# Kernel tuning notes

Measured on AMD Instinct MI355X. Metric: run time of the kernel, lower is better.

The kernel has to match this reference:

```python
import jax, jax.numpy as jnp
import numpy as np

N_NODES = 120000
EM = 128
N_EDGES = 1920000
BS = 1024
L = 10

def setup_inputs() -> dict:
    key = jax.random.key(0)
    ks = jax.random.split(key, 24)
    stdv = 1.0 / np.sqrt(EM)
    u = lambda k, shape: jax.random.uniform(k, shape, jnp.float32, -stdv, stdv)
    return {
        'src': jax.random.randint(ks[0], (N_EDGES,), 0, N_NODES, jnp.int32),
        'dst': jax.random.randint(ks[1], (N_EDGES,), 0, N_NODES, jnp.int32),
        'user': jax.random.randint(ks[2], (BS, 1), 0, 20000, jnp.int32),
        'seq': jax.random.randint(ks[3], (BS, L), 0, 100000, jnp.int32),
        'mask': jnp.ones((BS, L), jnp.float32),
        'seq_len': jax.random.randint(ks[4], (BS,), 1, L, jnp.int32),
        'pos_idx': jax.random.randint(ks[5], (BS, L), 0, 200, jnp.int32),
        'item_num': 100000,
        'v2e': u(ks[6], (N_NODES, EM)),
        'W_self': u(ks[7], (EM, EM)),
        'W_neigh': u(ks[8], (EM, EM)),
        'sage_b': u(ks[9], (EM,)),
        'pos_emb': u(ks[10], (200, EM)),
        'w1': u(ks[11], (2 * EM, EM)),
        'w2': u(ks[12], (EM, 1)),
        'glu1_w': u(ks[13], (EM, EM)),
        'glu1_b': u(ks[14], (EM,)),
        'glu2_w': u(ks[15], (EM, EM)),
        'w3': u(ks[16], (EM, EM)),
        'w4': u(ks[17], (EM, 1)),
        'glu3_w': u(ks[18], (EM, EM)),
        'glu3_b': u(ks[19], (EM,)),
        'glu4_w': u(ks[20], (EM, EM)),
        'sc_w': u(ks[21], (2 * EM, 1)),
        'sc_b': u(ks[22], (1,)),
    }


def reference(src, dst, user, seq, mask, seq_len, pos_idx, item_num,
              v2e, W_self, W_neigh, sage_b, pos_emb,
              w1, w2, glu1_w, glu1_b, glu2_w,
              w3, w4, glu3_w, glu3_b, glu4_w, sc_w, sc_b):
    N = v2e.shape[0]
    # SAGEConv 'mean': fc_self(x) + fc_neigh(mean over in-neighbors) + bias, then ReLU
    deg = jax.ops.segment_sum(jnp.ones_like(dst, jnp.float32), dst, num_segments=N)
    agg = jax.ops.segment_sum(v2e[src], dst, num_segments=N)
    agg = agg / jnp.clip(deg, 1.0)[:, None]
    h1 = jax.nn.relu(v2e @ W_self + agg @ W_neigh + sage_b)

    u_idx = user + item_num                      # [bs,1]
    node_embeds = (h1[seq] + v2e[seq]) * 0.5     # [bs,L,em]
    user_embeds = (h1[u_idx] + v2e[u_idx]) * 0.5 # [bs,1,em]
    seq_embeds = user_embeds[:, 0]               # [bs,em]

    m = mask[..., None]                          # [bs,L,1]
    # compute_hidden_vector (GLU-gated attention with positional embedding)
    pe = pos_emb[pos_idx]                        # [bs,L,em]
    tmp = jnp.sum(node_embeds * m, axis=1) / jnp.sum(m, axis=1)  # masked mean [bs,em]
    hs = tmp[:, None, :]
    nh = jnp.tanh(jnp.concatenate([pe, node_embeds], -1) @ w1)
    nh = jax.nn.sigmoid(nh @ glu1_w + glu1_b + hs @ glu2_w)
    beta = (nh @ w2) * m
    sess_vec = jnp.sum(beta * node_embeds, axis=1)  # [bs,em]

    # sess_user_vector
    nh2 = jnp.tanh(node_embeds @ w3)
    nh2 = jax.nn.sigmoid(nh2 @ glu3_w + glu3_b + user_embeds @ glu4_w)
    beta2 = (nh2 @ w4) * m
    sess_user = jnp.sum(beta2 * node_embeds, axis=1)  # [bs,em]

    alpha = jax.nn.sigmoid(jnp.concatenate([sess_vec, sess_user], 1) @ sc_w + sc_b)  # [bs,1]
    seq_embeds = seq_embeds + alpha * sess_vec + (1.0 - alpha) * sess_user

    scores = seq_embeds @ v2e[1:].T              # [bs, N-1]
    return scores
```

## Files before the change

### kernel.cpp

```cpp
#include <hip/hip_runtime.h>
#include <stdint.h>

#define N_NODES   120000
#define EM        128
#define N_EDGES_C 1920000
#define BSZ       1024
#define SL        10
#define N_GATHER  (BSZ*SL + BSZ)
#define N_OUTCOL  (N_NODES - 1)
#define NBLK_E    1875
#define CHUNK_E   1024
#define NPANEL    938
#define NBLK_S    (NPANEL*8)

typedef __attribute__((ext_vector_type(8))) short bf16x8;
typedef __attribute__((ext_vector_type(4))) float f32x4;

#define GLOBAL_AS __attribute__((address_space(1)))
#define LDS_AS    __attribute__((address_space(3)))

__device__ inline void gload_lds16(const void* g, void* l) {
  __builtin_amdgcn_global_load_lds((const GLOBAL_AS unsigned int*)g,
                                   (LDS_AS unsigned int*)l, 16, 0, 0);
}

__device__ inline unsigned pk_bf16(float a, float b) {
  unsigned ua = __builtin_bit_cast(unsigned, a);
  ua += 0x7fffu + ((ua >> 16) & 1u);
  unsigned ub = __builtin_bit_cast(unsigned, b);
  ub += 0x7fffu + ((ub >> 16) & 1u);
  return (ua >> 16) | (ub & 0xffff0000u);
}

__device__ inline float bf2f(unsigned short u) {
  return __builtin_bit_cast(float, ((unsigned)u) << 16);
}

#define MAP_OFF   0u
#define CNT_OFF   480000u
#define DEG_OFF   480256u
#define OFFS_OFF  525312u
#define CUR_OFF   570368u
#define AGG_OFF   615424u
#define SORT_OFF  21742592u
#define NE_OFF    29422592u
#define UE_OFF    34665472u
#define SB_OFF    35189760u
#define V2EB_OFF  37748736u

__global__ __launch_bounds__(256) void k_init(int* __restrict__ ws_ints) {
  int t = blockIdx.x*256 + threadIdx.x;
  ws_ints[t] = (t < N_NODES) ? -1 : 0;
}

__global__ __launch_bounds__(256) void k_tobf16(const float* __restrict__ v2e,
    unsigned short* __restrict__ v2eb) {
  size_t base = ((size_t)blockIdx.x*256 + threadIdx.x) * 8;
  float4 v0 = *(const float4*)(v2e + base);
  float4 v1 = *(const float4*)(v2e + base + 4);
  uint4 o;
  o.x = pk_bf16(v0.x, v0.y); o.y = pk_bf16(v0.z, v0.w);
  o.z = pk_bf16(v1.x, v1.y); o.w = pk_bf16(v1.z, v1.w);
  *(uint4*)(v2eb + base) = o;
}

__global__ __launch_bounds__(256) void k_assign(const int* __restrict__ seq,
    const int* __restrict__ user, const int* __restrict__ item_num,
    int* __restrict__ map, int* __restrict__ slotCount) {
  int t = blockIdx.x*256 + threadIdx.x;
  int idx = (t < BSZ*SL) ? seq[t] : (user[t - BSZ*SL] + item_num[0]);
  int old = atomicCAS(map + idx, -1, -2);
  if (old == -1) {
    int slot = atomicAdd(slotCount, 1);
    atomicExch(map + idx, slot);
  }
}

__global__ __launch_bounds__(256) void k_count(const int* __restrict__ dst,
    const int* __restrict__ map, int* __restrict__ deg_i) {
  int beg = blockIdx.x * CHUNK_E;
  #pragma unroll
  for (int it = 0; it < CHUNK_E/256; ++it) {
    int e = beg + it*256 + threadIdx.x;
    int slot = map[dst[e]];
    if (slot >= 0) atomicAdd(deg_i + slot, 1);
  }
}

__global__ __launch_bounds__(256) void k_scan(const int* __restrict__ deg_i,
    int* __restrict__ offs, int* __restrict__ cursor) {
  __shared__ int wsum[4];
  int tid = threadIdx.x;
  int lane = tid & 63, wv = tid >> 6;
  int carry = 0;
  for (int c = 0; c < N_GATHER/256; ++c) {
    int i = c*256 + tid;
    int v = deg_i[i];
    int s = v;
    #pragma unroll
    for (int o = 1; o < 64; o <<= 1) {
      int t = __shfl_up(s, o);
      if (lane >= o) s += t;
    }
    if (lane == 63) wsum[wv] = s;
    __syncthreads();
    int wbase = 0;
    #pragma unroll
    for (int q = 0; q < 4; ++q) if (q < wv) wbase += wsum[q];
    int tot = wsum[0] + wsum[1] + wsum[2] + wsum[3];
    int excl = s - v + wbase + carry;
    offs[i] = excl;
    cursor[i] = excl;
    carry += tot;
    __syncthreads();
  }
}

__global__ __launch_bounds__(256) void k_place(const int* __restrict__ src,
    const int* __restrict__ dst, const int* __restrict__ map,
    int* __restrict__ cursor, int* __restrict__ sorted) {
  int beg = blockIdx.x * CHUNK_E;
  #pragma unroll
  for (int it = 0; it < CHUNK_E/256; ++it) {
    int e = beg + it*256 + threadIdx.x;
    int slot = map[dst[e]];
    if (slot >= 0) {
      int pos = atomicAdd(cursor + slot, 1);
      sorted[pos] = src[e];
    }
  }
}

__global__ __launch_bounds__(256) void k_reduce(const unsigned short* __restrict__ v2eb,
    const int* __restrict__ offs, const int* __restrict__ deg_i,
    const int* __restrict__ slotCount, const int* __restrict__ sorted,
    float* __restrict__ agg) {
  int nslots = slotCount[0];
  int g = (blockIdx.x*blockDim.x + threadIdx.x) >> 5;
  int lg = threadIdx.x & 31;
  int ngrp = (gridDim.x*blockDim.x) >> 5;
  for (int slot = g; slot < nslots; slot += ngrp) {
    int beg = offs[slot];
    int end = beg + deg_i[slot];
    float a0 = 0.f, a1 = 0.f, a2 = 0.f, a3 = 0.f;
    for (int e = beg; e < end; ++e) {
      int s = sorted[e];
      ushort4 v = *(const ushort4*)(v2eb + (size_t)s*EM + lg*4);
      a0 += bf2f(v.x); a1 += bf2f(v.y); a2 += bf2f(v.z); a3 += bf2f(v.w);
    }
    *(float4*)(agg + (size_t)slot*EM + lg*4) = make_float4(a0, a1, a2, a3);
  }
}

__global__ __launch_bounds__(128) void k_embed(const int* __restrict__ seq,
    const int* __restrict__ user, const int* __restrict__ item_num,
    const int* __restrict__ map, const int* __restrict__ deg_i,
    const float* __restrict__ agg, const float* __restrict__ v2e,
    const float* __restrict__ W_self, const float* __restrict__ W_neigh,
    const float* __restrict__ sage_b,
    float* __restrict__ node_emb, float* __restrict__ user_emb) {
  __shared__ float xs[8][EM];
  __shared__ float xa[8][EM];
  int j = threadIdx.x;
  int base = blockIdx.x * 8;
  #pragma unroll
  for (int r = 0; r < 8; ++r) {
    int rg = base + r;
    int idx = (rg < BSZ*SL) ? seq[rg] : (user[rg - BSZ*SL] + item_num[0]);
    int slot = map[idx];
    float rd = 1.0f / fmaxf((float)deg_i[slot], 1.0f);
    xs[r][j] = v2e[(size_t)idx*EM + j];
    xa[r][j] = agg[(size_t)slot*EM + j] * rd;
  }
  __syncthreads();
  float acc[8] = {0.f,0.f,0.f,0.f,0.f,0.f,0.f,0.f};
  for (int k = 0; k < EM; ++k) {
    float a  = W_self[k*EM + j];
    float bb = W_neigh[k*EM + j];
    #pragma unroll
    for (int r = 0; r < 8; ++r) acc[r] += xs[r][k]*a + xa[r][k]*bb;
  }
  float bias = sage_b[j];
  #pragma unroll
  for (int r = 0; r < 8; ++r) {
    int rg = base + r;
    float h = fmaxf(acc[r] + bias, 0.0f);
    float emb = 0.5f * (h + xs[r][j]);
    if (rg < BSZ*SL) node_emb[(size_t)rg*EM + j] = emb;
    else             user_emb[(size_t)(rg - BSZ*SL)*EM + j] = emb;
  }
}

__global__ __launch_bounds__(128) void k_session(
    const float* __restrict__ node_emb, const float* __restrict__ user_emb,
    const int* __restrict__ pos_idx, const float* __restrict__ mask_in,
    const float* __restrict__ pos_emb,
    const float* __restrict__ w1, const float* __restrict__ w2,
    const float* __restrict__ glu1_w, const float* __restrict__ glu1_b,
    const float* __restrict__ glu2_w,
    const float* __restrict__ w3, const float* __restrict__ w4,
    const float* __restrict__ glu3_w, const float* __restrict__ glu3_b,
    const float* __restrict__ glu4_w,
    const float* __restrict__ sc_w, const float* __restrict__ sc_b,
    unsigned short* __restrict__ seqb) {
  __shared__ float ne[SL][EM], pe[SL][EM], r1[SL][EM], r2[SL][EM];
  __shared__ float ue[EM], hsS[EM], redA[EM];
  __shared__ float mls[SL], bl1[SL], bl2[SL];
  __shared__ float alphaS;
  int b = blockIdx.x, j = threadIdx.x;
  ue[j] = user_emb[b*EM + j];
  if (j < SL) mls[j] = mask_in[b*SL + j];
  #pragma unroll
  for (int l = 0; l < SL; ++l) {
    ne[l][j] = node_emb[(size_t)(b*SL + l)*EM + j];
    int p = pos_idx[b*SL + l];
    pe[l][j] = pos_emb[(size_t)p*EM + j];
  }
  __syncthreads();
  float s = 0.f, ms = 0.f;
  #pragma unroll
  for (int l = 0; l < SL; ++l) { s += mls[l]*ne[l][j]; ms += mls[l]; }
  hsS[j] = s / ms;
  float a1[SL], a2[SL];
  #pragma unroll
  for (int l = 0; l < SL; ++l) { a1[l] = 0.f; a2[l] = 0.f; }
  for (int k = 0; k < EM; ++k) {
    float wt  = w1[k*EM + j];
    float wb  = w1[(k+EM)*EM + j];
    float w3v = w3[k*EM + j];
    #pragma unroll
    for (int l = 0; l < SL; ++l) {
      a1[l] += pe[l][k]*wt + ne[l][k]*wb;
      a2[l] += ne[l][k]*w3v;
    }
  }
  #pragma unroll
  for (int l = 0; l < SL; ++l) { r1[l][j] = tanhf(a1[l]); r2[l][j] = tanhf(a2[l]); }
  __syncthreads();
  float g1[SL], g2[SL];
  #pragma unroll
  for (int l = 0; l < SL; ++l) { g1[l] = 0.f; g2[l] = 0.f; }
  float hsa = 0.f, uea = 0.f;
  for (int k = 0; k < EM; ++k) {
    float c1 = glu1_w[k*EM + j];
    float c2 = glu2_w[k*EM + j];
    float c3 = glu3_w[k*EM + j];
    float c4 = glu4_w[k*EM + j];
    hsa += hsS[k]*c2;
    uea += ue[k]*c4;
    #pragma unroll
    for (int l = 0; l < SL; ++l) {
      g1[l] += r1[l][k]*c1;
      g2[l] += r2[l][k]*c3;
    }
  }
  float b1 = glu1_b[j], b3 = glu3_b[j];
  float w2v = w2[j], w4v = w4[j];
  __syncthreads();
  #pragma unroll
  for (int l = 0; l < SL; ++l) {
    float s1 = 1.f/(1.f + expf(-(g1[l] + b1 + hsa)));
    float s2 = 1.f/(1.f + expf(-(g2[l] + b3 + uea)));
    r1[l][j] = s1 * w2v;
    r2[l][j] = s2 * w4v;
  }
  __syncthreads();
  if (j < SL) {
    float t1 = 0.f, t2 = 0.f;
    for (int t = 0; t < EM; ++t) { t1 += r1[j][t]; t2 += r2[j][t]; }
    bl1[j] = t1 * mls[j];
    bl2[j] = t2 * mls[j];
  }
  __syncthreads();
  float sv = 0.f, su = 0.f;
  #pragma unroll
  for (int l = 0; l < SL; ++l) { sv += bl1[l]*ne[l][j]; su += bl2[l]*ne[l][j]; }
  redA[j] = sv*sc_w[j] + su*sc_w[EM + j];
  __syncthreads();
  if (j == 0) {
    float t = 0.f;
    for (int k = 0; k < EM; ++k) t += redA[k];
    alphaS = 1.f/(1.f + expf(-(t + sc_b[0])));
  }
  __syncthreads();
  float al = alphaS;
  float val = ue[j] + al*sv + (1.f - al)*su;
  unsigned uv = __builtin_bit_cast(unsigned, val);
  uv += 0x7fffu + ((uv >> 16) & 1u);
  seqb[b*EM + j] = (unsigned short)(uv >> 16);
}

__global__ __launch_bounds__(256, 3) void k_scores(
    const unsigned short* __restrict__ seqb,
    const unsigned short* __restrict__ v2eb, float* __restrict__ out) {
  __shared__ char Bs[32768];
  __shared__ float scr[4][16][68];
  int tid = threadIdx.x;
  int bid = blockIdx.x;
  int lid = (bid & 7) * (NBLK_S/8) + (bid >> 3);
  int m0 = (lid & 7) * 128;
  int n0 = (lid >> 3) * 128;
  int w = tid >> 6, lane = tid & 63;
  const char* v2eb_c = (const char*)v2eb;
  #pragma unroll
  for (int i = 0; i < 8; ++i) {
    int chunk = i*4 + w;
    int o = chunk*1024 + lane*16;
    int row = o >> 8;
    int c = o & 255;
    int rowg = n0 + 1 + row;
    if (rowg > N_OUTCOL) rowg = N_OUTCOL;
    const void* src = v2eb_c + (size_t)rowg*256 + (c ^ ((row & 7) << 4));
    gload_lds16(src, Bs + chunk*1024);
  }
  asm volatile("s_waitcnt vmcnt(0)");
  __syncthreads();

  int wm = w >> 1, wn = w & 1;
  int lr = lane & 15, lg = lane >> 4;
  f32x4 acc[4][4];
  #pragma unroll
  for (int mi = 0; mi < 4; ++mi)
    #pragma unroll
    for (int ni = 0; ni < 4; ++ni)
      acc[mi][ni] = 0.f;
  #pragma unroll
  for (int ks = 0; ks < 4; ++ks) {
    bf16x8 a[4], bfr[4];
    #pragma unroll
    for (int mi = 0; mi < 4; ++mi)
      a[mi] = *(const bf16x8*)(seqb + (size_t)(m0 + wm*64 + mi*16 + lr)*EM + ks*32 + lg*8);
    #pragma unroll
    for (int ni = 0; ni < 4; ++ni) {
      int row = wn*64 + ni*16 + lr;
      int off = (row*256 + ks*64 + lg*16) ^ ((row & 7) << 4);
      bfr[ni] = *(const bf16x8*)(Bs + off);
    }
    #pragma unroll
    for (int mi = 0; mi < 4; ++mi)
      #pragma unroll
      for (int ni = 0; ni < 4; ++ni)
        acc[mi][ni] = __builtin_amdgcn_mfma_f32_16x16x32_bf16(a[mi], bfr[ni], acc[mi][ni], 0, 0, 0);
  }

  float (*sw)[68] = scr[w];
  int nbase = n0 + wn*64;
  #pragma unroll
  for (int mi = 0; mi < 4; ++mi) {
    #pragma unroll
    for (int ni = 0; ni < 4; ++ni)
      #pragma unroll
      for (int r = 0; r < 4; ++r)
        sw[lg*4 + r][ni*16 + lr] = acc[mi][ni][r];
    asm volatile("s_waitcnt lgkmcnt(0)" ::: "memory");
    #pragma unroll
    for (int q = 0; q < 4; ++q) {
      int row16 = q*4 + lg;
      float4 v = *(const float4*)&sw[row16][lr*4];
      int m = m0 + wm*64 + mi*16 + row16;
      int nc = nbase + lr*4;
      size_t base = (size_t)m * N_OUTCOL + nc;
      if (nc + 3 < N_OUTCOL) {
        *(float4*)(out + base) = v;
      } else if (nc < N_OUTCOL) {
        float vv[4] = {v.x, v.y, v.z, v.w};
        #pragma unroll
        for (int t = 0; t < 4; ++t)
          if (nc + t < N_OUTCOL) out[base + t] = vv[t];
      }
    }
    asm volatile("s_waitcnt lgkmcnt(0)" ::: "memory");
  }
}

extern "C" void kernel_launch(void* const* d_in, const int* in_sizes, int n_in,
                              void* d_out, int out_size, void* d_ws, size_t ws_size,
                              hipStream_t stream) {
  const int*   src      = (const int*)d_in[0];
  const int*   dst      = (const int*)d_in[1];
  const int*   user     = (const int*)d_in[2];
  const int*   seq      = (const int*)d_in[3];
  const float* mask     = (const float*)d_in[4];
  const int*   pos_idx  = (const int*)d_in[6];
  const int*   item_num = (const int*)d_in[7];
  const float* v2e      = (const float*)d_in[8];
  const float* W_self   = (const float*)d_in[9];
  const float* W_neigh  = (const float*)d_in[10];
  const float* sage_b   = (const float*)d_in[11];
  const float* pos_emb  = (const float*)d_in[12];
  const float* w1       = (const float*)d_in[13];
  const float* w2       = (const float*)d_in[14];
  const float* glu1_w   = (const float*)d_in[15];
  const float* glu1_b   = (const float*)d_in[16];
  const float* glu2_w   = (const float*)d_in[17];
  const float* w3       = (const float*)d_in[18];
  const float* w4       = (const float*)d_in[19];
  const float* glu3_w   = (const float*)d_in[20];
  const float* glu3_b   = (const float*)d_in[21];
  const float* glu4_w   = (const float*)d_in[22];
  const float* sc_w     = (const float*)d_in[23];
  const float* sc_b     = (const float*)d_in[24];
  float* out = (float*)d_out;
  char*  ws  = (char*)d_ws;

  int*   map       = (int*)(ws + MAP_OFF);
  int*   slotCount = (int*)(ws + CNT_OFF);
  int*   deg_i     = (int*)(ws + DEG_OFF);
  int*   offs      = (int*)(ws + OFFS_OFF);
  int*   cursor    = (int*)(ws + CUR_OFF);
  float* agg       = (float*)(ws + AGG_OFF);
  int*   sorted    = (int*)(ws + SORT_OFF);
  float* node_emb  = (float*)(ws + NE_OFF);
  float* user_emb  = (float*)(ws + UE_OFF);
  unsigned short* seqb  = (unsigned short*)(ws + SB_OFF);
  unsigned short* v2eb  = (unsigned short*)(ws + V2EB_OFF);

  k_init<<<513, 256, 0, stream>>>((int*)ws);
  k_tobf16<<<7500, 256, 0, stream>>>(v2e, v2eb);
  k_assign<<<N_GATHER/256, 256, 0, stream>>>(seq, user, item_num, map, slotCount);
  k_count<<<NBLK_E, 256, 0, stream>>>(dst, map, deg_i);
  k_scan<<<1, 256, 0, stream>>>(deg_i, offs, cursor);
  k_place<<<NBLK_E, 256, 0, stream>>>(src, dst, map, cursor, sorted);
  k_reduce<<<1408, 256, 0, stream>>>(v2eb, offs, deg_i, slotCount, sorted, agg);
  k_embed<<<N_GATHER/8, 128, 0, stream>>>(seq, user, item_num, map, deg_i, agg, v2e,
                                          W_self, W_neigh, sage_b, node_emb, user_emb);
  k_session<<<BSZ, 128, 0, stream>>>(node_emb, user_emb, pos_idx, mask, pos_emb,
      w1, w2, glu1_w, glu1_b, glu2_w, w3, w4, glu3_w, glu3_b, glu4_w, sc_w, sc_b, seqb);
  k_scores<<<NBLK_S, 256, 0, stream>>>(seqb, v2eb, out);
}
```

Measured before the change: 398.6 us.

## Make scores kernel persistent over four N-tiles with prefetch overlapping stores

Each scores block now walks four consecutive 128-column tiles of v2e instead of one, so the grid is a quarter of its former size. The next tile's global-to-LDS load is issued after the MFMA loop and overlaps the epilogue that writes the output. This is meant to cut per-block launch and load latency and hide B-tile fetch behind the write-bound epilogue. The cost is fewer blocks (1880) and added barriers, which may reduce parallelism on the GPU.

```diff
diff --git a/kernel.cpp b/kernel.cpp
--- a/kernel.cpp
+++ b/kernel.cpp
@@ -10,8 +10,8 @@
 #define N_OUTCOL  (N_NODES - 1)
 #define NBLK_E    1875
 #define CHUNK_E   1024
-#define NPANEL    938
-#define NBLK_S    (NPANEL*8)
+#define NPANEL4   235
+#define NBLK_S4   (NPANEL4*8)
 
 typedef __attribute__((ext_vector_type(8))) short bf16x8;
 typedef __attribute__((ext_vector_type(4))) float f32x4;
@@ -297,79 +297,105 @@
   __shared__ float scr[4][16][68];
   int tid = threadIdx.x;
   int bid = blockIdx.x;
-  int lid = (bid & 7) * (NBLK_S/8) + (bid >> 3);
+  int lid = (bid & 7) * NPANEL4 + (bid >> 3);
   int m0 = (lid & 7) * 128;
-  int n0 = (lid >> 3) * 128;
+  int p4 = lid >> 3;
   int w = tid >> 6, lane = tid & 63;
+  int wm = w >> 1, wn = w & 1;
+  int lr = lane & 15, lg = lane >> 4;
   const char* v2eb_c = (const char*)v2eb;
+
+  int srow[8], scol[8], schunk[8];
   #pragma unroll
   for (int i = 0; i < 8; ++i) {
     int chunk = i*4 + w;
     int o = chunk*1024 + lane*16;
-    int row = o >> 8;
-    int c = o & 255;
-    int rowg = n0 + 1 + row;
-    if (rowg > N_OUTCOL) rowg = N_OUTCOL;
-    const void* src = v2eb_c + (size_t)rowg*256 + (c ^ ((row & 7) << 4));
-    gload_lds16(src, Bs + chunk*1024);
+    srow[i] = o >> 8;
+    scol[i] = (o & 255) ^ ((srow[i] & 7) << 4);
+    schunk[i] = chunk;
+  }
+
+  {
+    int nb = p4*512 + 0*128;
+    #pragma unroll
+    for (int i = 0; i < 8; ++i) {
+      int rowg = nb + 1 + srow[i];
+      if (rowg > N_OUTCOL) rowg = N_OUTCOL;
+      gload_lds16(v2eb_c + (size_t)rowg*256 + scol[i], Bs + schunk[i]*1024);
+    }
   }
   asm volatile("s_waitcnt vmcnt(0)");
   __syncthreads();
 
-  int wm = w >> 1, wn = w & 1;
-  int lr = lane & 15, lg = lane >> 4;
-  f32x4 acc[4][4];
-  #pragma unroll
-  for (int mi = 0; mi < 4; ++mi)
-    #pragma unroll
-    for (int ni = 0; ni < 4; ++ni)
-      acc[mi][ni] = 0.f;
-  #pragma unroll
-  for (int ks = 0; ks < 4; ++ks) {
-    bf16x8 a[4], bfr[4];
+  float (*sw)[68] = scr[w];
+  #pragma unroll 1
+  for (int t = 0; t < 4; ++t) {
+    int n0 = p4*512 + t*128;
+    f32x4 acc[4][4];
     #pragma unroll
     for (int mi = 0; mi < 4; ++mi)
-      a[mi] = *(const bf16x8*)(seqb + (size_t)(m0 + wm*64 + mi*16 + lr)*EM + ks*32 + lg*8);
-    #pragma unroll
-    for (int ni = 0; ni < 4; ++ni) {
-      int row = wn*64 + ni*16 + lr;
-      int off = (row*256 + ks*64 + lg*16) ^ ((row & 7) << 4);
-      bfr[ni] = *(const bf16x8*)(Bs + off);
-    }
-    #pragma unroll
-    for (int mi = 0; mi < 4; ++mi)
       #pragma unroll
       for (int ni = 0; ni < 4; ++ni)
-        acc[mi][ni] = __builtin_amdgcn_mfma_f32_16x16x32_bf16(a[mi], bfr[ni], acc[mi][ni], 0, 0, 0);
-  }
-
-  float (*sw)[68] = scr[w];
-  int nbase = n0 + wn*64;
-  #pragma unroll
-  for (int mi = 0; mi < 4; ++mi) {
-    #pragma unroll
-    for (int ni = 0; ni < 4; ++ni)
-      #pragma unroll
-      for (int r = 0; r < 4; ++r)
-        sw[lg*4 + r][ni*16 + lr] = acc[mi][ni][r];
-    asm volatile("s_waitcnt lgkmcnt(0)" ::: "memory");
-    #pragma unroll
-    for (int q = 0; q < 4; ++q) {
-      int row16 = q*4 + lg;
-      float4 v = *(const float4*)&sw[row16][lr*4];
-      int m = m0 + wm*64 + mi*16 + row16;
-      int nc = nbase + lr*4;
-      size_t base = (size_t)m * N_OUTCOL + nc;
-      if (nc + 3 < N_OUTCOL) {
-        *(float4*)(out + base) = v;
-      } else if (nc < N_OUTCOL) {
-        float vv[4] = {v.x, v.y, v.z, v.w};
+        acc[mi][ni] = 0.f;
+    #pragma unroll
+    for (int ks = 0; ks < 4; ++ks) {
+      bf16x8 a[4], bfr[4];
+      #pragma unroll
+      for (int mi = 0; mi < 4; ++mi)
+        a[mi] = *(const bf16x8*)(seqb + (size_t)(m0 + wm*64 + mi*16 + lr)*EM + ks*32 + lg*8);
+      #pragma unroll
+      for (int ni = 0; ni < 4; ++ni) {
+        int row = wn*64 + ni*16 + lr;
+        int off = (row*256 + ks*64 + lg*16) ^ ((row & 7) << 4);
+        bfr[ni] = *(const bf16x8*)(Bs + off);
+      }
+      #pragma unroll
+      for (int mi = 0; mi < 4; ++mi)
         #pragma unroll
-        for (int t = 0; t < 4; ++t)
-          if (nc + t < N_OUTCOL) out[base + t] = vv[t];
+        for (int ni = 0; ni < 4; ++ni)
+          acc[mi][ni] = __builtin_amdgcn_mfma_f32_16x16x32_bf16(a[mi], bfr[ni], acc[mi][ni], 0, 0, 0);
+    }
+    __syncthreads();
+    if (t < 3) {
+      int nb = p4*512 + (t+1)*128;
+      #pragma unroll
+      for (int i = 0; i < 8; ++i) {
+        int rowg = nb + 1 + srow[i];
+        if (rowg > N_OUTCOL) rowg = N_OUTCOL;
+        gload_lds16(v2eb_c + (size_t)rowg*256 + scol[i], Bs + schunk[i]*1024);
       }
     }
-    asm volatile("s_waitcnt lgkmcnt(0)" ::: "memory");
+    int nbase = n0 + wn*64;
+    #pragma unroll
+    for (int mi = 0; mi < 4; ++mi) {
+      #pragma unroll
+      for (int ni = 0; ni < 4; ++ni)
+        #pragma unroll
+        for (int r = 0; r < 4; ++r)
+          sw[lg*4 + r][ni*16 + lr] = acc[mi][ni][r];
+      asm volatile("s_waitcnt lgkmcnt(0)" ::: "memory");
+      #pragma unroll
+      for (int q = 0; q < 4; ++q) {
+        int row16 = q*4 + lg;
+        float4 v = *(const float4*)&sw[row16][lr*4];
+        int m = m0 + wm*64 + mi*16 + row16;
+        int nc = nbase + lr*4;
+        size_t base = (size_t)m * N_OUTCOL + nc;
+        if (nc + 3 < N_OUTCOL) {
+          *(float4*)(out + base) = v;
+        } else if (nc < N_OUTCOL) {
+          float vv[4] = {v.x, v.y, v.z, v.w};
+          #pragma unroll
+          for (int tt = 0; tt < 4; ++tt)
+            if (nc + tt < N_OUTCOL) out[base + tt] = vv[tt];
+        }
+      }
+      asm volatile("s_waitcnt lgkmcnt(0)" ::: "memory");
+    }
+    if (t < 3) {
+      asm volatile("s_waitcnt vmcnt(0)");
+      __syncthreads();
+    }
   }
 }
 
@@ -426,5 +452,5 @@
                                           W_self, W_neigh, sage_b, node_emb, user_emb);
   k_session<<<BSZ, 128, 0, stream>>>(node_emb, user_emb, pos_idx, mask, pos_emb,
       w1, w2, glu1_w, glu1_b, glu2_w, w3, w4, glu3_w, glu3_b, glu4_w, sc_w, sc_b, seqb);
-  k_scores<<<NBLK_S, 256, 0, stream>>>(seqb, v2eb, out);
-}
+  k_scores<<<NBLK_S4, 256, 0, stream>>>(seqb, v2eb, out);
+}
```

New measurement: 519.4 us. 30.3% more time.
